# Kernel tuning notes

Measured on AMD Instinct MI355X. Metric: run time of the kernel, lower is better.

## Reference

```python
import jax, jax.numpy as jnp
import numpy as np

TOP_K = 2  # module default top_k


def setup_inputs() -> dict:
    key = jax.random.key(0)
    k1, k2, k3 = jax.random.split(key, 3)
    B, D, E = 4096, 1024, 64  # tokens, input_dim, num_experts
    return {
        "tensor1": jax.random.normal(k1, (B, D), dtype=jnp.float32),
        "tensor2": jax.random.normal(k2, (B, D), dtype=jnp.float32),
        "gate_weight": jax.random.normal(k3, (E, 2 * D), dtype=jnp.float32) * 0.02,
    }


def reference(tensor1, tensor2, gate_weight):
    # x: (B, 2D)
    x = jnp.concatenate((tensor1, tensor2), axis=-1)
    # pairwise L2 distance between each token and each expert vector
    diff = gate_weight[None, :, :] - x[:, None, :]          # (B, E, 2D)
    logits = -jnp.sqrt(jnp.sum(diff * diff, axis=-1))        # (B, E)
    topk_logits, indices = jax.lax.top_k(logits, TOP_K)      # (B, K)
    gating_weights = jax.nn.softmax(topk_logits, axis=-1)    # (B, K)
    rows = jnp.arange(logits.shape[0])[:, None]              # (B, 1)
    sparse_gating = jnp.zeros_like(logits).at[rows, indices].set(gating_weights)
    return sparse_gating
```

## Files before the change

### kernel.cpp

```cpp
#include <hip/hip_runtime.h>
#include <math.h>

#define NTOK 4096
#define NDIM 1024
#define KTOT 2048
#define NEXP 64
#define NWAVE 16
#define KCH  (KTOT / NWAVE)
#define NSTEP (KCH / 32)
#define RS   68

typedef _Float16 half8 __attribute__((ext_vector_type(8)));
typedef float    floatx4 __attribute__((ext_vector_type(4)));

#define XSCALE 16.0f
#define WSCALE 1024.0f
#define INVSCALE (1.0f / (16.0f * 1024.0f))

struct h2pair { _Float16 h, l; };
__device__ __forceinline__ h2pair split2(float v) {
    h2pair r;
    r.h = (_Float16)v;
    r.l = (_Float16)(v - (float)r.h);
    return r;
}

__global__ __launch_bounds__(256) void prep_w(const float* __restrict__ W,
                                              _Float16* __restrict__ WhT,
                                              _Float16* __restrict__ WlT,
                                              float* __restrict__ nrm) {
    const int e = blockIdx.x, t = threadIdx.x;
    const float* row = W + (size_t)e * KTOT + t * 8;
    const float4 a = *reinterpret_cast<const float4*>(row);
    const float4 b = *reinterpret_cast<const float4*>(row + 4);
    float ss = fmaf(a.x, a.x, fmaf(a.y, a.y, fmaf(a.z, a.z, fmaf(a.w, a.w, 0.f))));
    ss = fmaf(b.x, b.x, fmaf(b.y, b.y, fmaf(b.z, b.z, fmaf(b.w, b.w, ss))));

    const h2pair p0 = split2(a.x * WSCALE), p1 = split2(a.y * WSCALE);
    const h2pair p2 = split2(a.z * WSCALE), p3 = split2(a.w * WSCALE);
    const h2pair p4 = split2(b.x * WSCALE), p5 = split2(b.y * WSCALE);
    const h2pair p6 = split2(b.z * WSCALE), p7 = split2(b.w * WSCALE);
    half8 h, l;
    h[0]=p0.h; h[1]=p1.h; h[2]=p2.h; h[3]=p3.h; h[4]=p4.h; h[5]=p5.h; h[6]=p6.h; h[7]=p7.h;
    l[0]=p0.l; l[1]=p1.l; l[2]=p2.l; l[3]=p3.l; l[4]=p4.l; l[5]=p5.l; l[6]=p6.l; l[7]=p7.l;
    const size_t idx = ((size_t)t * NEXP + e) * 8;
    *reinterpret_cast<half8*>(WhT + idx) = h;
    *reinterpret_cast<half8*>(WlT + idx) = l;

    #pragma unroll
    for (int off = 32; off > 0; off >>= 1) ss += __shfl_down(ss, off, 64);
    __shared__ float red[4];
    const int lane = t & 63, wv = t >> 6;
    if (lane == 0) red[wv] = ss;
    __syncthreads();
    if (t == 0) nrm[e] = (red[0] + red[1]) + (red[2] + red[3]);
}

__global__ __launch_bounds__(1024) void gate_fused(const float* __restrict__ t1,
                                                   const float* __restrict__ t2,
                                                   const _Float16* __restrict__ WhT,
                                                   const _Float16* __restrict__ WlT,
                                                   const float* __restrict__ nrm,
                                                   float* __restrict__ out) {
    __shared__ float Sd[NWAVE][16 * RS];
    __shared__ float Cn[NWAVE][16];

    const int tid  = threadIdx.x;
    const int lane = tid & 63;
    const int wv   = tid >> 6;
    const int tok0 = blockIdx.x * 16;
    const int kbase = wv * KCH;
    const int n  = lane & 15;
    const int fq = lane >> 4;

    const float* __restrict__ xb = ((kbase < NDIM)
        ? (t1 + (size_t)(tok0 + n) * NDIM + kbase)
        : (t2 + (size_t)(tok0 + n) * NDIM + (kbase - NDIM))) + fq * 8;
    const _Float16* __restrict__ whb = WhT + ((size_t)(kbase >> 3) + fq) * (NEXP * 8) + n * 8;
    const _Float16* __restrict__ wlb = WlT + ((size_t)(kbase >> 3) + fq) * (NEXP * 8) + n * 8;

    floatx4 acc[4];
    #pragma unroll
    for (int j = 0; j < 4; ++j) { acc[j][0]=0.f; acc[j][1]=0.f; acc[j][2]=0.f; acc[j][3]=0.f; }
    float ssx0 = 0.f, ssx1 = 0.f;

    #pragma unroll
    for (int s = 0; s < NSTEP; ++s) {
        const float4 x0 = *reinterpret_cast<const float4*>(xb + s * 32);
        const float4 x1 = *reinterpret_cast<const float4*>(xb + s * 32 + 4);
        half8 bh[4], bl[4];
        #pragma unroll
        for (int j = 0; j < 4; ++j) {
            bh[j] = *reinterpret_cast<const half8*>(whb + (size_t)s * 4 * (NEXP * 8) + j * 128);
            bl[j] = *reinterpret_cast<const half8*>(wlb + (size_t)s * 4 * (NEXP * 8) + j * 128);
        }
        ssx0 = fmaf(x0.x, x0.x, fmaf(x0.y, x0.y, fmaf(x0.z, x0.z, fmaf(x0.w, x0.w, ssx0))));
        ssx1 = fmaf(x1.x, x1.x, fmaf(x1.y, x1.y, fmaf(x1.z, x1.z, fmaf(x1.w, x1.w, ssx1))));
        const h2pair q0 = split2(x0.x * XSCALE), q1 = split2(x0.y * XSCALE);
        const h2pair q2 = split2(x0.z * XSCALE), q3 = split2(x0.w * XSCALE);
        const h2pair q4 = split2(x1.x * XSCALE), q5 = split2(x1.y * XSCALE);
        const h2pair q6 = split2(x1.z * XSCALE), q7 = split2(x1.w * XSCALE);
        half8 ah, al;
        ah[0]=q0.h; ah[1]=q1.h; ah[2]=q2.h; ah[3]=q3.h; ah[4]=q4.h; ah[5]=q5.h; ah[6]=q6.h; ah[7]=q7.h;
        al[0]=q0.l; al[1]=q1.l; al[2]=q2.l; al[3]=q3.l; al[4]=q4.l; al[5]=q5.l; al[6]=q6.l; al[7]=q7.l;
        #pragma unroll
        for (int j = 0; j < 4; ++j)
            acc[j] = __builtin_amdgcn_mfma_f32_16x16x32_f16(ah, bh[j], acc[j], 0, 0, 0);
        #pragma unroll
        for (int j = 0; j < 4; ++j)
            acc[j] = __builtin_amdgcn_mfma_f32_16x16x32_f16(al, bh[j], acc[j], 0, 0, 0);
        #pragma unroll
        for (int j = 0; j < 4; ++j)
            acc[j] = __builtin_amdgcn_mfma_f32_16x16x32_f16(ah, bl[j], acc[j], 0, 0, 0);
    }

    #pragma unroll
    for (int j = 0; j < 4; ++j) {
        #pragma unroll
        for (int i = 0; i < 4; ++i)
            Sd[wv][(fq * 4 + i) * RS + 16 * j + n] = acc[j][i];
    }
    float ssx = ssx0 + ssx1;
    ssx += __shfl_xor(ssx, 16, 64);
    ssx += __shfl_xor(ssx, 32, 64);
    if (lane < 16) Cn[wv][lane] = ssx;
    __syncthreads();

    {
        const int t = wv;
        float gsum = 0.f, csum = 0.f;
        #pragma unroll
        for (int w = 0; w < NWAVE; ++w) {
            gsum += Sd[w][t * RS + lane];
            csum += Cn[w][t];
        }
        const float S = fmaf(-2.f * INVSCALE, gsum, csum) + nrm[lane];
        const float logit = -sqrtf(S);

        float v1 = logit; int i1 = lane;
        #pragma unroll
        for (int off = 32; off > 0; off >>= 1) {
            float ov = __shfl_xor(v1, off, 64);
            int   oi = __shfl_xor(i1, off, 64);
            if (ov > v1 || (ov == v1 && oi < i1)) { v1 = ov; i1 = oi; }
        }
        float v2 = (lane == i1) ? -__builtin_inff() : logit;
        int   i2 = lane;
        #pragma unroll
        for (int off = 32; off > 0; off >>= 1) {
            float ov = __shfl_xor(v2, off, 64);
            int   oi = __shfl_xor(i2, off, 64);
            if (ov > v2 || (ov == v2 && oi < i2)) { v2 = ov; i2 = oi; }
        }
        const float e2  = expf(v2 - v1);
        const float inv = 1.f / (1.f + e2);
        const float o = (lane == i1) ? inv : ((lane == i2) ? e2 * inv : 0.f);
        out[(size_t)(tok0 + t) * NEXP + lane] = o;
    }
}

extern "C" void kernel_launch(void* const* d_in, const int* in_sizes, int n_in,
                              void* d_out, int out_size, void* d_ws, size_t ws_size,
                              hipStream_t stream) {
    const float* t1 = (const float*)d_in[0];
    const float* t2 = (const float*)d_in[1];
    const float* W  = (const float*)d_in[2];
    float* out = (float*)d_out;

    char* ws = (char*)d_ws;
    float*    nrm = (float*)ws;
    _Float16* WhT = (_Float16*)(nrm + NEXP);
    _Float16* WlT = WhT + (size_t)NEXP * KTOT;

    prep_w<<<NEXP, 256, 0, stream>>>(W, WhT, WlT, nrm);
    gate_fused<<<NTOK / 16, 1024, 0, stream>>>(t1, t2, WhT, WlT, nrm, out);
}
```

Measured before the change: 86.33 us.

## Fuse weight prep into gating kernel and halve waves per block

Drops the separate prep_w launch. Each block now reads the fp32 gate weights directly and does the fp16 hi/lo split and the squared-norm reduction inline. The block shrinks from 16 to 8 waves, so each wave covers twice the K range and finalises two tokens. This removes a kernel launch and the workspace round-trip. In exchange, all 256 blocks redo the weight conversion, read twice as many weight bytes (fp32 instead of two fp16 halves), and run more VALU work per MFMA step.

```diff
diff --git a/kernel.cpp b/kernel.cpp
--- a/kernel.cpp
+++ b/kernel.cpp
@@ -5,7 +5,7 @@
 #define NDIM 1024
 #define KTOT 2048
 #define NEXP 64
-#define NWAVE 16
+#define NWAVE 8
 #define KCH  (KTOT / NWAVE)
 #define NSTEP (KCH / 32)
 #define RS   68
@@ -25,45 +25,13 @@
     return r;
 }
 
-__global__ __launch_bounds__(256) void prep_w(const float* __restrict__ W,
-                                              _Float16* __restrict__ WhT,
-                                              _Float16* __restrict__ WlT,
-                                              float* __restrict__ nrm) {
-    const int e = blockIdx.x, t = threadIdx.x;
-    const float* row = W + (size_t)e * KTOT + t * 8;
-    const float4 a = *reinterpret_cast<const float4*>(row);
-    const float4 b = *reinterpret_cast<const float4*>(row + 4);
-    float ss = fmaf(a.x, a.x, fmaf(a.y, a.y, fmaf(a.z, a.z, fmaf(a.w, a.w, 0.f))));
-    ss = fmaf(b.x, b.x, fmaf(b.y, b.y, fmaf(b.z, b.z, fmaf(b.w, b.w, ss))));
-
-    const h2pair p0 = split2(a.x * WSCALE), p1 = split2(a.y * WSCALE);
-    const h2pair p2 = split2(a.z * WSCALE), p3 = split2(a.w * WSCALE);
-    const h2pair p4 = split2(b.x * WSCALE), p5 = split2(b.y * WSCALE);
-    const h2pair p6 = split2(b.z * WSCALE), p7 = split2(b.w * WSCALE);
-    half8 h, l;
-    h[0]=p0.h; h[1]=p1.h; h[2]=p2.h; h[3]=p3.h; h[4]=p4.h; h[5]=p5.h; h[6]=p6.h; h[7]=p7.h;
-    l[0]=p0.l; l[1]=p1.l; l[2]=p2.l; l[3]=p3.l; l[4]=p4.l; l[5]=p5.l; l[6]=p6.l; l[7]=p7.l;
-    const size_t idx = ((size_t)t * NEXP + e) * 8;
-    *reinterpret_cast<half8*>(WhT + idx) = h;
-    *reinterpret_cast<half8*>(WlT + idx) = l;
-
-    #pragma unroll
-    for (int off = 32; off > 0; off >>= 1) ss += __shfl_down(ss, off, 64);
-    __shared__ float red[4];
-    const int lane = t & 63, wv = t >> 6;
-    if (lane == 0) red[wv] = ss;
-    __syncthreads();
-    if (t == 0) nrm[e] = (red[0] + red[1]) + (red[2] + red[3]);
-}
-
-__global__ __launch_bounds__(1024) void gate_fused(const float* __restrict__ t1,
-                                                   const float* __restrict__ t2,
-                                                   const _Float16* __restrict__ WhT,
-                                                   const _Float16* __restrict__ WlT,
-                                                   const float* __restrict__ nrm,
-                                                   float* __restrict__ out) {
+__global__ __launch_bounds__(512) void gate_all(const float* __restrict__ t1,
+                                                const float* __restrict__ t2,
+                                                const float* __restrict__ W,
+                                                float* __restrict__ out) {
     __shared__ float Sd[NWAVE][16 * RS];
     __shared__ float Cn[NWAVE][16];
+    __shared__ float Wn[NWAVE][NEXP];
 
     const int tid  = threadIdx.x;
     const int lane = tid & 63;
@@ -76,13 +44,13 @@
     const float* __restrict__ xb = ((kbase < NDIM)
         ? (t1 + (size_t)(tok0 + n) * NDIM + kbase)
         : (t2 + (size_t)(tok0 + n) * NDIM + (kbase - NDIM))) + fq * 8;
-    const _Float16* __restrict__ whb = WhT + ((size_t)(kbase >> 3) + fq) * (NEXP * 8) + n * 8;
-    const _Float16* __restrict__ wlb = WlT + ((size_t)(kbase >> 3) + fq) * (NEXP * 8) + n * 8;
+    const float* __restrict__ wb = W + kbase + fq * 8 + (size_t)n * KTOT;
 
     floatx4 acc[4];
     #pragma unroll
     for (int j = 0; j < 4; ++j) { acc[j][0]=0.f; acc[j][1]=0.f; acc[j][2]=0.f; acc[j][3]=0.f; }
     float ssx0 = 0.f, ssx1 = 0.f;
+    float wss[4] = {0.f, 0.f, 0.f, 0.f};
 
     #pragma unroll
     for (int s = 0; s < NSTEP; ++s) {
@@ -91,8 +59,19 @@
         half8 bh[4], bl[4];
         #pragma unroll
         for (int j = 0; j < 4; ++j) {
-            bh[j] = *reinterpret_cast<const half8*>(whb + (size_t)s * 4 * (NEXP * 8) + j * 128);
-            bl[j] = *reinterpret_cast<const half8*>(wlb + (size_t)s * 4 * (NEXP * 8) + j * 128);
+            const float* wp = wb + (size_t)j * 16 * KTOT + s * 32;
+            const float4 wa = *reinterpret_cast<const float4*>(wp);
+            const float4 wc = *reinterpret_cast<const float4*>(wp + 4);
+            wss[j] = fmaf(wa.x, wa.x, fmaf(wa.y, wa.y, fmaf(wa.z, wa.z, fmaf(wa.w, wa.w, wss[j]))));
+            wss[j] = fmaf(wc.x, wc.x, fmaf(wc.y, wc.y, fmaf(wc.z, wc.z, fmaf(wc.w, wc.w, wss[j]))));
+            const h2pair p0 = split2(wa.x * WSCALE), p1 = split2(wa.y * WSCALE);
+            const h2pair p2 = split2(wa.z * WSCALE), p3 = split2(wa.w * WSCALE);
+            const h2pair p4 = split2(wc.x * WSCALE), p5 = split2(wc.y * WSCALE);
+            const h2pair p6 = split2(wc.z * WSCALE), p7 = split2(wc.w * WSCALE);
+            bh[j][0]=p0.h; bh[j][1]=p1.h; bh[j][2]=p2.h; bh[j][3]=p3.h;
+            bh[j][4]=p4.h; bh[j][5]=p5.h; bh[j][6]=p6.h; bh[j][7]=p7.h;
+            bl[j][0]=p0.l; bl[j][1]=p1.l; bl[j][2]=p2.l; bl[j][3]=p3.l;
+            bl[j][4]=p4.l; bl[j][5]=p5.l; bl[j][6]=p6.l; bl[j][7]=p7.l;
         }
         ssx0 = fmaf(x0.x, x0.x, fmaf(x0.y, x0.y, fmaf(x0.z, x0.z, fmaf(x0.w, x0.w, ssx0))));
         ssx1 = fmaf(x1.x, x1.x, fmaf(x1.y, x1.y, fmaf(x1.z, x1.z, fmaf(x1.w, x1.w, ssx1))));
@@ -124,17 +103,28 @@
     ssx += __shfl_xor(ssx, 16, 64);
     ssx += __shfl_xor(ssx, 32, 64);
     if (lane < 16) Cn[wv][lane] = ssx;
+    #pragma unroll
+    for (int j = 0; j < 4; ++j) {
+        wss[j] += __shfl_xor(wss[j], 16, 64);
+        wss[j] += __shfl_xor(wss[j], 32, 64);
+    }
+    if (fq == 0) {
+        #pragma unroll
+        for (int j = 0; j < 4; ++j) Wn[wv][16 * j + n] = wss[j];
+    }
     __syncthreads();
 
-    {
-        const int t = wv;
-        float gsum = 0.f, csum = 0.f;
+    #pragma unroll
+    for (int tt = 0; tt < 2; ++tt) {
+        const int t = wv * 2 + tt;
+        float gsum = 0.f, csum = 0.f, wsum = 0.f;
         #pragma unroll
         for (int w = 0; w < NWAVE; ++w) {
             gsum += Sd[w][t * RS + lane];
             csum += Cn[w][t];
+            wsum += Wn[w][lane];
         }
-        const float S = fmaf(-2.f * INVSCALE, gsum, csum) + nrm[lane];
+        const float S = fmaf(-2.f * INVSCALE, gsum, csum) + wsum;
         const float logit = -sqrtf(S);
 
         float v1 = logit; int i1 = lane;
@@ -166,12 +156,7 @@
     const float* t2 = (const float*)d_in[1];
     const float* W  = (const float*)d_in[2];
     float* out = (float*)d_out;
+    (void)d_ws; (void)ws_size;
 
-    char* ws = (char*)d_ws;
-    float*    nrm = (float*)ws;
-    _Float16* WhT = (_Float16*)(nrm + NEXP);
-    _Float16* WlT = WhT + (size_t)NEXP * KTOT;
-
-    prep_w<<<NEXP, 256, 0, stream>>>(W, WhT, WlT, nrm);
-    gate_fused<<<NTOK / 16, 1024, 0, stream>>>(t1, t2, WhT, WlT, nrm, out);
+    gate_all<<<NTOK / 16, 512, 0, stream>>>(t1, t2, W, out);
 }
```

Result: slower. 107.4 us (+24.4%).
